# Optimization experiments

Measured on AMD Instinct MI355X. Metric: run time of the kernel, lower is better.

The kernel has to match this reference:

```python
import jax, jax.numpy as jnp
import numpy as np

PRE_NMS_TOP_K = 6000   # 'test' mode
POST_NMS_TOP_K = 300   # 'test' mode
IOU_THRESHOLD = 0.7


def setup_inputs() -> dict:
    key = jax.random.key(0)
    k1, k2, k3, k4 = jax.random.split(key, 4)
    B, A, H, W = 1, 9, 64, 96
    N = H * W * A  # 55296 anchors
    pred_cls = jax.random.normal(k1, (B, 2 * A, H, W), dtype=jnp.float32)
    pred_loc = jax.random.normal(k2, (B, 4 * A, H, W), dtype=jnp.float32) * 0.1
    # anchors in normalized (cx, cy, w, h) format
    cxcy = jax.random.uniform(k3, (N, 2), dtype=jnp.float32)
    wh = jax.random.uniform(k4, (N, 2), dtype=jnp.float32) * 0.2 + 0.02
    anchor = jnp.concatenate([cxcy, wh], axis=-1)
    return {"pred_cls": pred_cls, "pred_loc": pred_loc, "anchor": anchor}


def _decode_to_xy(loc, anchor):
    # decode: t(cx,cy) * a(w,h) + a(cx,cy); exp(t(w,h)) * a(w,h); then cxcy -> xyxy
    cxcy = loc[:, :2] * anchor[:, 2:] + anchor[:, :2]
    wh = jnp.exp(loc[:, 2:]) * anchor[:, 2:]
    return jnp.concatenate([cxcy - wh * 0.5, cxcy + wh * 0.5], axis=-1)


def _iou_matrix(boxes):
    # boxes: [N,4] xyxy -> [N,N] IoU
    area = (boxes[:, 2] - boxes[:, 0]) * (boxes[:, 3] - boxes[:, 1])
    lt = jnp.maximum(boxes[:, None, :2], boxes[None, :, :2])  # [N,N,2]
    rb = jnp.minimum(boxes[:, None, 2:], boxes[None, :, 2:])  # [N,N,2]
    wh = jnp.clip(rb - lt, 0.0)
    inter = wh[..., 0] * wh[..., 1]
    union = area[:, None] + area[None, :] - inter
    return inter / jnp.maximum(union, 1e-12)


def _nms_keep(boxes, iou_threshold):
    # boxes already sorted by descending score -> greedy NMS
    n = boxes.shape[0]
    iou = _iou_matrix(boxes)
    idx = jnp.arange(n)

    def body(i, keep):
        suppress = (iou[i] > iou_threshold) & (idx > i)
        return jnp.where(keep[i], keep & ~suppress, keep)

    return jax.lax.fori_loop(0, n, body, jnp.ones((n,), dtype=bool))


def reference(pred_cls, pred_loc, anchor):
    B = pred_cls.shape[0]
    # NCHW -> NHWC -> [N, 2] / [N, 4]  (batch squeezed, B == 1)
    cls = jnp.transpose(pred_cls, (0, 2, 3, 1)).reshape(B, -1, 2)[0]
    loc = jnp.transpose(pred_loc, (0, 2, 3, 1)).reshape(B, -1, 4)[0]

    roi = jnp.clip(_decode_to_xy(loc, anchor), 0.0, 1.0)           # [N,4]
    scores = jax.nn.sigmoid(cls)[:, 1]                              # [N]

    order = jnp.argsort(-scores)[:PRE_NMS_TOP_K]                    # descending
    roi = roi[order]                                                # [K,4]

    keep = _nms_keep(roi, IOU_THRESHOLD)                            # [K] bool
    # kept boxes first (stable -> preserves score order), take top 300
    sel = jnp.argsort(jnp.where(keep, 0, 1), stable=True)[:POST_NMS_TOP_K]
    valid = keep[sel]
    # pad with zeros if fewer than 300 boxes survive NMS (torch returns a
    # dynamically-sized tensor; we keep a fixed [300,4] with zero padding)
    return jnp.where(valid[:, None], roi[sel], 0.0)
```

## Files before the change

### kernel.cpp

```cpp
#include <hip/hip_runtime.h>


#define ADIM 9
#define NANCH 55296
#define HWSZ 6144
#define CH_U4 1536
#define TOT_U4 13824
#define SAMP_U4 3456
#define TOPK 6000
#define OUTK 300
#define NBINS 16384
#define CAP 8192
#define SCAP 1024
#define SRANK 128
#define MROWS 512
#define MW 8
#define THR 0.7f

typedef unsigned long long u64;
typedef unsigned int u32;

__device__ __forceinline__ u32 flipu(u32 b) {
    u32 u = (b & 0x80000000u) ? ~b : (b | 0x80000000u);
    return ~u;
}

__device__ __forceinline__ bool iou_gt(float4 a, float aa, float4 b, float ba) {
    float ix = fminf(a.z, b.z) - fmaxf(a.x, b.x);
    float iy = fminf(a.w, b.w) - fmaxf(a.y, b.y);
    float inter = fmaxf(ix, 0.f) * fmaxf(iy, 0.f);
    float u = fmaxf(aa + ba - inter, 1e-12f);
    float d = __builtin_fmaf(-THR, u, inter);
    if (__builtin_fabsf(d) > 1e-6f * u) return d > 0.f;
    return inter / u > THR;
}

__device__ __forceinline__ float4 decode_box(const float* __restrict__ loc,
                                             const float* __restrict__ anc, u32 n) {
    u32 a = n % 9u, hw = n / 9u;
    float t0 = loc[(4 * a + 0) * HWSZ + hw];
    float t1 = loc[(4 * a + 1) * HWSZ + hw];
    float t2 = loc[(4 * a + 2) * HWSZ + hw];
    float t3 = loc[(4 * a + 3) * HWSZ + hw];
    float4 an = reinterpret_cast<const float4*>(anc)[n];
    float cx = t0 * an.z + an.x;
    float cy = t1 * an.w + an.y;
    float bw = expf(t2) * an.z;
    float bh = expf(t3) * an.w;
    return make_float4(fminf(fmaxf(cx - bw * 0.5f, 0.f), 1.f),
                       fminf(fmaxf(cy - bh * 0.5f, 0.f), 1.f),
                       fminf(fmaxf(cx + bw * 0.5f, 0.f), 1.f),
                       fminf(fmaxf(cy + bh * 0.5f, 0.f), 1.f));
}

__device__ __forceinline__ u64 sx64(u64 v, int m) {
    u32 lo = __shfl_xor((u32)(v & 0xffffffffu), m, 64);
    u32 hi = __shfl_xor((u32)(v >> 32), m, 64);
    return ((u64)hi << 32) | lo;
}

__device__ __forceinline__ u64 ce64(u64 v, int j, int lane, bool up) {
    u64 pv = sx64(v, j);
    u64 mn = (pv < v) ? pv : v;
    u64 mx = (pv < v) ? v : pv;
    return (((lane & j) == 0) == up) ? mn : mx;
}

__device__ __forceinline__ uint4 ld_cls4(const uint4* __restrict__ cls4, int i) {
    int ch = i / CH_U4;
    int e4 = i - ch * CH_U4;
    return cls4[(2 * ch + 1) * CH_U4 + e4];
}

__device__ __forceinline__ u32 block_scan(u32 s, int wid, int lane, u32* wsum) {
    u32 x = s;
    #pragma unroll
    for (int d = 1; d < 64; d <<= 1) {
        u32 y = __shfl_up(x, (unsigned)d, 64);
        if (lane >= d) x += y;
    }
    if (lane == 63) wsum[wid] = x;
    __syncthreads();
    if (wid == 0) {
        u32 w = (lane < 16) ? wsum[lane] : 0u;
        #pragma unroll
        for (int d = 1; d < 16; d <<= 1) {
            u32 y = __shfl_up(w, (unsigned)d, 64);
            if (lane >= d) w += y;
        }
        if (lane < 16) wsum[lane] = w;
    }
    __syncthreads();
    return x + (wid ? wsum[wid - 1] : 0u);
}

__device__ __forceinline__ u32 find_cutoff(const u32* hist, u32 thresh, int tid,
                                           int wid, int lane, u32* wsum, u32* sB) {
    u32 h[16];
    const uint4* h4 = reinterpret_cast<const uint4*>(hist);
    #pragma unroll
    for (int k = 0; k < 4; ++k) {
        uint4 v = h4[tid * 4 + k];
        h[4 * k + 0] = v.x; h[4 * k + 1] = v.y; h[4 * k + 2] = v.z; h[4 * k + 3] = v.w;
    }
    u32 s = 0;
    #pragma unroll
    for (int b = 0; b < 16; ++b) s += h[b];
    u32 incl = block_scan(s, wid, lane, wsum);
    u32 before = incl - s;
    if (before < thresh && incl >= thresh) {
        u32 run = before;
        #pragma unroll
        for (int b = 0; b < 16; ++b) {
            run += h[b];
            if (run >= thresh) { sB[0] = (u32)(tid * 16 + b); break; }
        }
    }
    __syncthreads();
    u32 r = sB[0];
    __syncthreads();
    return r;
}

__global__ void __launch_bounds__(1024) k_scan(const float* __restrict__ cls,
                                               u32* __restrict__ wsSfs,
                                               u32* __restrict__ wsSidx,
                                               u32* __restrict__ wsMeta) {
    __shared__ u32 hist[NBINS];
    __shared__ __align__(16) u32 sfs[SCAP];
    __shared__ u32 sidx[SCAP];
    __shared__ u32 wsum[16];
    __shared__ u32 sB[2];
    __shared__ u32 shu[2];

    const int tid = threadIdx.x;
    const int wid = tid >> 6;
    const int lane = tid & 63;
    const uint4* cls4 = reinterpret_cast<const uint4*>(cls);

    u64* h64 = (u64*)hist;
    for (int i = tid; i < NBINS / 2; i += 1024) h64[i] = 0ull;
    if (tid < 2) shu[tid] = 0;
    __syncthreads();
    {
        uint4 s0 = ld_cls4(cls4, 4 * tid);
        uint4 s1 = ld_cls4(cls4, 4 * (tid + 1024));
        uint4 s2 = ld_cls4(cls4, 4 * (tid + 2048));
        bool has3 = tid < (SAMP_U4 - 3072);
        uint4 s3 = has3 ? ld_cls4(cls4, 4 * (tid + 3072)) : make_uint4(0u,0u,0u,0u);
        atomicAdd(&hist[flipu(s0.x) >> 18], 1u); atomicAdd(&hist[flipu(s0.y) >> 18], 1u);
        atomicAdd(&hist[flipu(s0.z) >> 18], 1u); atomicAdd(&hist[flipu(s0.w) >> 18], 1u);
        atomicAdd(&hist[flipu(s1.x) >> 18], 1u); atomicAdd(&hist[flipu(s1.y) >> 18], 1u);
        atomicAdd(&hist[flipu(s1.z) >> 18], 1u); atomicAdd(&hist[flipu(s1.w) >> 18], 1u);
        atomicAdd(&hist[flipu(s2.x) >> 18], 1u); atomicAdd(&hist[flipu(s2.y) >> 18], 1u);
        atomicAdd(&hist[flipu(s2.z) >> 18], 1u); atomicAdd(&hist[flipu(s2.w) >> 18], 1u);
        if (has3) {
            atomicAdd(&hist[flipu(s3.x) >> 18], 1u); atomicAdd(&hist[flipu(s3.y) >> 18], 1u);
            atomicAdd(&hist[flipu(s3.z) >> 18], 1u); atomicAdd(&hist[flipu(s3.w) >> 18], 1u);
        }
    }
    __syncthreads();
    const u32 B1 = find_cutoff(hist, SRANK, tid, wid, lane, wsum, sB);
    const u32 K1 = (B1 + 1u) << 18;

    u64 bm = 0;
    u32 cnt = 0;
    #pragma unroll
    for (int half = 0; half < 2; ++half) {
        uint4 buf[7];
        #pragma unroll
        for (int kk = 0; kk < 7; ++kk) {
            int i = (half * 7 + kk) * 1024 + tid;
            buf[kk] = (i < TOT_U4) ? ld_cls4(cls4, i) : make_uint4(0xFFFFFFFFu,0xFFFFFFFFu,0xFFFFFFFFu,0xFFFFFFFFu);
        }
        #pragma unroll
        for (int kk = 0; kk < 7; ++kk) {
            int i = (half * 7 + kk) * 1024 + tid;
            if (i < TOT_U4) {
                #pragma unroll
                for (int c = 0; c < 4; ++c) {
                    u32 b = (c == 0) ? buf[kk].x : (c == 1) ? buf[kk].y
                          : (c == 2) ? buf[kk].z : buf[kk].w;
                    if (flipu(b) < K1) {
                        cnt++;
                        bm |= 1ull << ((half * 7 + kk) * 4 + c);
                    }
                }
            }
        }
    }
    u32 incl = block_scan(cnt, wid, lane, wsum);
    u32 base = incl - cnt;
    if (tid == 1023) shu[0] = incl;
    __syncthreads();
    const u32 csRaw = shu[0];
    const u32 cs = csRaw < SCAP ? csRaw : SCAP;
    if (csRaw <= SCAP) {
        u64 m = bm;
        u32 o = base;
        while (m) {
            int b = __ffsll((unsigned long long)m) - 1;
            m &= m - 1;
            int kk = b >> 2, c = b & 3;
            int i = kk * 1024 + tid;
            uint4 v = ld_cls4(cls4, i);
            u32 raw = (c == 0) ? v.x : (c == 1) ? v.y : (c == 2) ? v.z : v.w;
            int ch = i / CH_U4;
            int e4 = i - ch * CH_U4;
            u32 n = (u32)((e4 * 4 + c) * ADIM + ch);
            if (o < SCAP) { sfs[o] = flipu(raw); sidx[o] = n; }
            o++;
        }
    }
    if (tid >= (int)cs) { sfs[tid] = 0xFFFFFFFFu; sidx[tid] = 0xFFFFFFFFu; }
    __syncthreads();
    wsSfs[tid] = sfs[tid];
    wsSidx[tid] = sidx[tid];
    if (tid == 0) { wsMeta[0] = csRaw; wsMeta[1] = B1; }
}

__global__ void __launch_bounds__(1024) k_rank(const float* __restrict__ loc,
                                               const float* __restrict__ anc,
                                               const u32* __restrict__ wsSfs,
                                               const u32* __restrict__ wsSidx,
                                               const u32* __restrict__ wsMeta,
                                               float4* __restrict__ boxS,
                                               float* __restrict__ areaS) {
    __shared__ u32 Lfs[SCAP];
    __shared__ u32 Lidx[SCAP];
    const int tid = threadIdx.x;
    const u32 csRaw = wsMeta[0];
    if (csRaw > SCAP) return;

    Lfs[tid] = wsSfs[tid];
    Lidx[tid] = wsSidx[tid];
    __syncthreads();

    const int ci = blockIdx.x * 64 + (tid >> 4);
    const int p = tid & 15;
    const u32 myf = Lfs[ci];
    const u32 myi = Lidx[ci];
    u32 r = 0;
    #pragma unroll 8
    for (int k = 0; k < 64; ++k) {
        int j = k * 16 + p;
        u32 fj = Lfs[j];
        u32 ij = Lidx[j];
        r += (fj < myf) || (fj == myf && ij < myi);
    }
    r += __shfl_xor(r, 1, 64);
    r += __shfl_xor(r, 2, 64);
    r += __shfl_xor(r, 4, 64);
    r += __shfl_xor(r, 8, 64);
    if (p == 0 && (u32)ci < csRaw) {
        float4 b = decode_box(loc, anc, myi);
        boxS[r] = b;
        areaS[r] = (b.z - b.x) * (b.w - b.y);
    }
}

__global__ void __launch_bounds__(1024) k_mat(const u32* __restrict__ wsMeta,
                                              const float4* __restrict__ boxS,
                                              const float* __restrict__ areaS,
                                              u32* __restrict__ maskG32) {
    __shared__ float4 B[MROWS];
    __shared__ float  A[MROWS];
    __shared__ u32 M32[32][16];
    const int tid = threadIdx.x;
    const u32 csRaw = wsMeta[0];
    if (csRaw > SCAP) return;
    const u32 rowsv = csRaw < MROWS ? csRaw : MROWS;

    if (tid < MROWS) { B[tid] = boxS[tid]; A[tid] = areaS[tid]; }
    if (tid < 512) M32[tid >> 4][tid & 15] = 0u;
    __syncthreads();

    const int rl = tid >> 5;
    const int sub = tid & 31;
    const int row = blockIdx.x + 16 * rl;
    if (row < (int)rowsv) {
        const int j0 = sub * 16;
        int jmax = row < j0 + 16 ? row : j0 + 16;
        if (j0 < jmax) {
            float4 rb = B[row];
            float rba = A[row];
            u32 bits = 0;
            #pragma unroll 4
            for (int j = j0; j < jmax; ++j)
                if (iou_gt(rb, rba, B[j], A[j])) bits |= 1u << (j - j0);
            if (bits) atomicOr(&M32[rl][sub >> 1], bits << ((sub & 1) * 16));
        }
    }
    __syncthreads();
    if (tid < 512) {
        int rl2 = tid >> 4, w = tid & 15;
        int row2 = blockIdx.x + 16 * rl2;
        maskG32[row2 * 16 + w] = M32[rl2][w];
    }
}

__global__ void __launch_bounds__(1024) k_greedy(const float* __restrict__ cls,
                                                 const float* __restrict__ loc,
                                                 const float* __restrict__ anc,
                                                 const u32* __restrict__ wsMeta,
                                                 const float4* __restrict__ boxS,
                                                 const float* __restrict__ areaS,
                                                 const u32* __restrict__ maskG32,
                                                 float4* __restrict__ out) {
    __shared__ u64 cand[CAP];
    __shared__ u64 smask[MROWS][MW];
    __shared__ float4 sbox[SCAP];
    __shared__ float  sarea[SCAP];
    __shared__ float4 kept[OUTK];
    __shared__ float  karea[OUTK];
    __shared__ float4 cbox[64];
    __shared__ float  carea[64];
    __shared__ u64 supw[16];
    __shared__ u64 sbyp[1024];
    __shared__ u32 wsum[16];
    __shared__ u32 sB[2];
    __shared__ u32 shu[8];

    const int tid = threadIdx.x;
    const int wid = tid >> 6;
    const int lane = tid & 63;
    u32* hist = (u32*)cand;
    const uint4* cls4 = reinterpret_cast<const uint4*>(cls);

    const u32 csRaw = wsMeta[0];
    const u32 cs = csRaw < SCAP ? csRaw : SCAP;
    const bool fast = (csRaw <= SCAP);

    if (tid < 8) shu[tid] = 0;
    sbox[tid] = boxS[tid];
    sarea[tid] = areaS[tid];
    {
        u32* sm32 = (u32*)smask;
        #pragma unroll
        for (int k = 0; k < 8; ++k) sm32[k * 1024 + tid] = maskG32[k * 1024 + tid];
    }
    __syncthreads();

    if (fast) {
        const u32 rowsv = cs < MROWS ? cs : MROWS;
        if (wid == 0) {
            u32 kc = 0, nexti0 = 0;
            u64 K[MW];
            #pragma unroll
            for (int w = 0; w < MW; ++w) K[w] = 0ull;
            #pragma unroll
            for (int cw = 0; cw < MW; ++cw) {
                u32 i0 = (u32)cw * 64u;
                if (i0 < rowsv && kc < OUTK) {
                    u32 ci = i0 + (u32)lane;
                    bool valid = ci < rowsv;
                    u64 myw[MW];
                    #pragma unroll
                    for (int w = 0; w < MW; ++w) myw[w] = valid ? smask[ci][w] : 0ull;
                    u64 supk = 0;
                    #pragma unroll
                    for (int w = 0; w < MW; ++w) supk |= myw[w] & K[w];
                    bool ia = valid && (supk == 0ull);
                    u64 inch = myw[cw] & ((1ull << lane) - 1ull);
                    u64 A = __ballot(ia ? 1 : 0);
                    for (int itx = 0; itx < 64; ++itx) {
                        bool na = ia && ((inch & A) == 0ull);
                        u64 A2 = __ballot(na ? 1 : 0);
                        if (A2 == A) break;
                        A = A2;
                    }
                    bool kp = (A >> lane) & 1;
                    u32 rank = (u32)__popcll(A & ((1ull << lane) - 1ull));
                    if (kp && kc + rank < OUTK) {
                        float4 c = sbox[ci];
                        kept[kc + rank] = c;
                        karea[kc + rank] = sarea[ci];
                        out[kc + rank] = c;
                    }
                    K[cw] = A;
                    kc += (u32)__popcll(A);
                    nexti0 = i0 + 64;
                }
            }
            if (lane == 0) {
                shu[4] = kc > OUTK ? OUTK : kc;
                shu[5] = nexti0;
            }
        }

        const u32 limit = cs;
        while (true) {
            __syncthreads();
            u32 kc = shu[4], i0 = shu[5];
            if (kc >= OUTK || i0 >= limit) break;
            u32 ci = i0 + (u32)lane;
            bool valid = ci < limit;
            float4 c = sbox[valid ? ci : 0];
            float ca = sarea[valid ? ci : 0];

            bool sup = false;
            for (u32 j = (u32)wid; j < kc; j += 16)
                sup = sup || iou_gt(c, ca, kept[j], karea[j]);
            u64 bal = __ballot(sup ? 1 : 0);
            if (lane == 0) supw[wid] = bal;

            u64 sby = 0;
            u32 smax = 4u * wid + 4u; if (smax > 63u) smax = 63u;
            for (u32 s = 4u * wid + 1u; s <= smax; ++s) {
                u32 p = ((u32)lane + s) & 63u;
                if (p < (u32)lane && (i0 + p) < limit)
                    if (iou_gt(c, ca, sbox[i0 + p], sarea[i0 + p])) sby |= (1ull << p);
            }
            sbyp[wid * 64 + lane] = sby;
            __syncthreads();

            if (wid == 0) {
                u64 sup64 = 0, sbyfull = 0;
                #pragma unroll
                for (int w = 0; w < 16; ++w) { sup64 |= supw[w]; sbyfull |= sbyp[w * 64 + lane]; }
                bool ia = valid && !((sup64 >> lane) & 1);
                u64 A = __ballot(ia ? 1 : 0);
                for (int itx = 0; itx < 64; ++itx) {
                    bool na = ia && ((sbyfull & A) == 0);
                    u64 A2 = __ballot(na ? 1 : 0);
                    if (A2 == A) break;
                    A = A2;
                }
                bool kp = (A >> lane) & 1;
                u32 rank = (u32)__popcll(A & ((1ull << lane) - 1ull));
                if (kp && kc + rank < OUTK) {
                    kept[kc + rank] = c; karea[kc + rank] = ca; out[kc + rank] = c;
                }
                if (lane == 0) {
                    u32 nk = kc + (u32)__popcll(A);
                    shu[4] = nk > OUTK ? OUTK : nk;
                    shu[5] = i0 + 64;
                }
            }
        }
    }

    __syncthreads();
    if (shu[4] < OUTK) {
        const u32 consumed = fast ? cs : 0u;
        u64* h64 = (u64*)hist;
        for (int i = tid; i < NBINS / 2; i += 1024) h64[i] = 0ull;
        __syncthreads();
        #pragma unroll
        for (int half = 0; half < 2; ++half) {
            uint4 buf[7];
            #pragma unroll
            for (int kk = 0; kk < 7; ++kk) {
                int i = (half * 7 + kk) * 1024 + tid;
                buf[kk] = (i < TOT_U4) ? ld_cls4(cls4, i) : make_uint4(0u,0u,0u,0u);
            }
            #pragma unroll
            for (int kk = 0; kk < 7; ++kk) {
                int i = (half * 7 + kk) * 1024 + tid;
                if (i < TOT_U4) {
                    atomicAdd(&hist[flipu(buf[kk].x) >> 18], 1u);
                    atomicAdd(&hist[flipu(buf[kk].y) >> 18], 1u);
                    atomicAdd(&hist[flipu(buf[kk].z) >> 18], 1u);
                    atomicAdd(&hist[flipu(buf[kk].w) >> 18], 1u);
                }
            }
        }
        __syncthreads();
        const u32 B2 = find_cutoff(hist, TOPK, tid, wid, lane, wsum, sB);
        u64 bm2 = 0;
        u32 cnt2 = 0;
        #pragma unroll
        for (int half = 0; half < 2; ++half) {
            uint4 buf[7];
            #pragma unroll
            for (int kk = 0; kk < 7; ++kk) {
                int i = (half * 7 + kk) * 1024 + tid;
                buf[kk] = (i < TOT_U4) ? ld_cls4(cls4, i) : make_uint4(0xFFFFFFFFu,0xFFFFFFFFu,0xFFFFFFFFu,0xFFFFFFFFu);
            }
            #pragma unroll
            for (int kk = 0; kk < 7; ++kk) {
                int i = (half * 7 + kk) * 1024 + tid;
                if (i < TOT_U4) {
                    #pragma unroll
                    for (int c = 0; c < 4; ++c) {
                        u32 b = (c == 0) ? buf[kk].x : (c == 1) ? buf[kk].y
                              : (c == 2) ? buf[kk].z : buf[kk].w;
                        if ((flipu(b) >> 18) <= B2) {
                            cnt2++;
                            bm2 |= 1ull << ((half * 7 + kk) * 4 + c);
                        }
                    }
                }
            }
        }
        __syncthreads();
        for (int i = tid; i < CAP; i += 1024) cand[i] = ~0ull;
        u32 incl2 = block_scan(cnt2, wid, lane, wsum);
        u32 base2 = incl2 - cnt2;
        if (tid == 1023) shu[1] = incl2;
        __syncthreads();
        {
            u64 m2 = bm2;
            u32 o = base2;
            while (m2) {
                int b = __ffsll((unsigned long long)m2) - 1;
                m2 &= m2 - 1;
                int kk = b >> 2, c = b & 3;
                int i = kk * 1024 + tid;
                uint4 v = ld_cls4(cls4, i);
                u32 raw = (c == 0) ? v.x : (c == 1) ? v.y : (c == 2) ? v.z : v.w;
                int ch = i / CH_U4;
                int e4 = i - ch * CH_U4;
                u32 n = (u32)((e4 * 4 + c) * ADIM + ch);
                if (o < CAP) cand[o] = ((u64)flipu(raw) << 32) | n;
                o++;
            }
        }
        __syncthreads();
        const u32 totF = shu[1];
        const u32 limfb = totF < TOPK ? totF : TOPK;
        for (int seg = wid; seg < CAP / 64; seg += 16) {
            u64 v = cand[seg * 64 + lane];
            #pragma unroll
            for (int k = 2; k <= 64; k <<= 1)
                #pragma unroll
                for (int j = k >> 1; j >= 1; j >>= 1)
                    v = ce64(v, j, lane, (((seg * 64 + lane) & k) == 0));
            cand[seg * 64 + lane] = v;
        }
        __syncthreads();
        for (int k = 128; k <= CAP; k <<= 1) {
            for (int j = k >> 1; j >= 64; j >>= 1) {
                for (u32 p = (u32)tid; p < CAP / 2; p += 1024) {
                    u32 i = ((p & ~(u32)(j - 1)) << 1) | (p & (u32)(j - 1));
                    u32 l = i | (u32)j;
                    bool up = ((i & (u32)k) == 0);
                    u64 a = cand[i], b = cand[l];
                    if ((a > b) == up) { cand[i] = b; cand[l] = a; }
                }
                __syncthreads();
            }
            for (int seg = wid; seg < CAP / 64; seg += 16) {
                u64 v = cand[seg * 64 + lane];
                bool up = (((seg * 64) & k) == 0);
                #pragma unroll
                for (int j = 32; j >= 1; j >>= 1) v = ce64(v, j, lane, up);
                cand[seg * 64 + lane] = v;
            }
            __syncthreads();
        }
        if (tid == 0) shu[5] = consumed;
        while (true) {
            __syncthreads();
            u32 kc = shu[4], i0 = shu[5];
            if (kc >= OUTK || i0 >= limfb) break;
            if (wid == 0) {
                u32 ci = i0 + (u32)lane;
                u32 n = (ci < limfb) ? (u32)cand[ci] : 0u;
                float4 b = decode_box(loc, anc, n);
                cbox[lane] = b;
                carea[lane] = (b.z - b.x) * (b.w - b.y);
            }
            __syncthreads();
            u32 ci = i0 + (u32)lane;
            bool valid = ci < limfb;
            float4 c = cbox[lane];
            float ca = carea[lane];
            bool sup = false;
            for (u32 j = (u32)wid; j < kc; j += 16)
                sup = sup || iou_gt(c, ca, kept[j], karea[j]);
            u64 bal = __ballot(sup ? 1 : 0);
            if (lane == 0) supw[wid] = bal;
            u64 sby = 0;
            u32 smax = 4u * wid + 4u; if (smax > 63u) smax = 63u;
            for (u32 s = 4u * wid + 1u; s <= smax; ++s) {
                u32 p = ((u32)lane + s) & 63u;
                if (p < (u32)lane && (i0 + p) < limfb)
                    if (iou_gt(c, ca, cbox[p], carea[p])) sby |= (1ull << p);
            }
            sbyp[wid * 64 + lane] = sby;
            __syncthreads();
            if (wid == 0) {
                u64 sup64 = 0, sbyfull = 0;
                #pragma unroll
                for (int w = 0; w < 16; ++w) { sup64 |= supw[w]; sbyfull |= sbyp[w * 64 + lane]; }
                bool ia = valid && !((sup64 >> lane) & 1);
                u64 A = __ballot(ia ? 1 : 0);
                for (int itx = 0; itx < 64; ++itx) {
                    bool na = ia && ((sbyfull & A) == 0);
                    u64 A2 = __ballot(na ? 1 : 0);
                    if (A2 == A) break;
                    A = A2;
                }
                bool kp = (A >> lane) & 1;
                u32 rank = (u32)__popcll(A & ((1ull << lane) - 1ull));
                if (kp && kc + rank < OUTK) {
                    kept[kc + rank] = c; karea[kc + rank] = ca; out[kc + rank] = c;
                }
                if (lane == 0) {
                    u32 nk = kc + (u32)__popcll(A);
                    shu[4] = nk > OUTK ? OUTK : nk;
                    shu[5] = i0 + 64;
                }
            }
        }
    }

    __syncthreads();
    u32 kc = shu[4];
    for (u32 r = (u32)tid; r < OUTK; r += 1024)
        if (r >= kc) out[r] = make_float4(0.f, 0.f, 0.f, 0.f);
}

extern "C" void kernel_launch(void* const* d_in, const int* in_sizes, int n_in,
                              void* d_out, int out_size, void* d_ws, size_t ws_size,
                              hipStream_t stream) {
    const float* cls = (const float*)d_in[0];
    const float* loc = (const float*)d_in[1];
    const float* anc = (const float*)d_in[2];

    char* ws = (char*)d_ws;
    u32*    wsSfs   = (u32*)(ws + 0);
    u32*    wsSidx  = (u32*)(ws + 4096);
    u32*    wsMeta  = (u32*)(ws + 8192);
    float4* boxS    = (float4*)(ws + 8208);
    float*  areaS   = (float*)(ws + 24592);
    u32*    maskG32 = (u32*)(ws + 28688);

    k_scan  <<<1, 1024, 0, stream>>>(cls, wsSfs, wsSidx, wsMeta);
    k_rank  <<<16, 1024, 0, stream>>>(loc, anc, wsSfs, wsSidx, wsMeta, boxS, areaS);
    k_mat   <<<16, 1024, 0, stream>>>(wsMeta, boxS, areaS, maskG32);
    k_greedy<<<1, 1024, 0, stream>>>(cls, loc, anc, wsMeta, boxS, areaS, maskG32, (float4*)d_out);
}
```

Baseline: 36.69 us.

## Fuse scan and rank kernels by recomputing the scan in every block

Merges the single-block candidate scan kernel and the 16-block rank kernel into one kernel launched with 16 blocks. Each block redundantly recomputes the histogram and candidate compaction, then ranks its own 64-candidate slice straight from shared memory. This removes one kernel launch and the global round trip of the candidate arrays. The cost is 16 copies of the full scan work competing for memory bandwidth.

```diff
diff --git a/kernel.cpp b/kernel.cpp
--- a/kernel.cpp
+++ b/kernel.cpp
@@ -122,10 +122,12 @@
     return r;
 }
 
-__global__ void __launch_bounds__(1024) k_scan(const float* __restrict__ cls,
-                                               u32* __restrict__ wsSfs,
-                                               u32* __restrict__ wsSidx,
-                                               u32* __restrict__ wsMeta) {
+__global__ void __launch_bounds__(1024) k_scanrank(const float* __restrict__ cls,
+                                                   const float* __restrict__ loc,
+                                                   const float* __restrict__ anc,
+                                                   u32* __restrict__ wsMeta,
+                                                   float4* __restrict__ boxS,
+                                                   float* __restrict__ areaS) {
     __shared__ u32 hist[NBINS];
     __shared__ __align__(16) u32 sfs[SCAP];
     __shared__ u32 sidx[SCAP];
@@ -195,7 +197,10 @@
     __syncthreads();
     const u32 csRaw = shu[0];
     const u32 cs = csRaw < SCAP ? csRaw : SCAP;
-    if (csRaw <= SCAP) {
+    if (blockIdx.x == 0 && tid == 0) { wsMeta[0] = csRaw; wsMeta[1] = B1; }
+    if (csRaw > SCAP) return;
+
+    {
         u64 m = bm;
         u32 o = base;
         while (m) {
@@ -214,38 +219,17 @@
     }
     if (tid >= (int)cs) { sfs[tid] = 0xFFFFFFFFu; sidx[tid] = 0xFFFFFFFFu; }
     __syncthreads();
-    wsSfs[tid] = sfs[tid];
-    wsSidx[tid] = sidx[tid];
-    if (tid == 0) { wsMeta[0] = csRaw; wsMeta[1] = B1; }
-}
-
-__global__ void __launch_bounds__(1024) k_rank(const float* __restrict__ loc,
-                                               const float* __restrict__ anc,
-                                               const u32* __restrict__ wsSfs,
-                                               const u32* __restrict__ wsSidx,
-                                               const u32* __restrict__ wsMeta,
-                                               float4* __restrict__ boxS,
-                                               float* __restrict__ areaS) {
-    __shared__ u32 Lfs[SCAP];
-    __shared__ u32 Lidx[SCAP];
-    const int tid = threadIdx.x;
-    const u32 csRaw = wsMeta[0];
-    if (csRaw > SCAP) return;
-
-    Lfs[tid] = wsSfs[tid];
-    Lidx[tid] = wsSidx[tid];
-    __syncthreads();
 
     const int ci = blockIdx.x * 64 + (tid >> 4);
     const int p = tid & 15;
-    const u32 myf = Lfs[ci];
-    const u32 myi = Lidx[ci];
+    const u32 myf = sfs[ci];
+    const u32 myi = sidx[ci];
     u32 r = 0;
     #pragma unroll 8
     for (int k = 0; k < 64; ++k) {
         int j = k * 16 + p;
-        u32 fj = Lfs[j];
-        u32 ij = Lidx[j];
+        u32 fj = sfs[j];
+        u32 ij = sidx[j];
         r += (fj < myf) || (fj == myf && ij < myi);
     }
     r += __shfl_xor(r, 1, 64);
@@ -620,15 +604,12 @@
     const float* anc = (const float*)d_in[2];
 
     char* ws = (char*)d_ws;
-    u32*    wsSfs   = (u32*)(ws + 0);
-    u32*    wsSidx  = (u32*)(ws + 4096);
-    u32*    wsMeta  = (u32*)(ws + 8192);
-    float4* boxS    = (float4*)(ws + 8208);
-    float*  areaS   = (float*)(ws + 24592);
-    u32*    maskG32 = (u32*)(ws + 28688);
-
-    k_scan  <<<1, 1024, 0, stream>>>(cls, wsSfs, wsSidx, wsMeta);
-    k_rank  <<<16, 1024, 0, stream>>>(loc, anc, wsSfs, wsSidx, wsMeta, boxS, areaS);
-    k_mat   <<<16, 1024, 0, stream>>>(wsMeta, boxS, areaS, maskG32);
-    k_greedy<<<1, 1024, 0, stream>>>(cls, loc, anc, wsMeta, boxS, areaS, maskG32, (float4*)d_out);
-}
+    u32*    wsMeta  = (u32*)(ws + 0);
+    float4* boxS    = (float4*)(ws + 16);
+    float*  areaS   = (float*)(ws + 16400);
+    u32*    maskG32 = (u32*)(ws + 20496);
+
+    k_scanrank<<<16, 1024, 0, stream>>>(cls, loc, anc, wsMeta, boxS, areaS);
+    k_mat     <<<16, 1024, 0, stream>>>(wsMeta, boxS, areaS, maskG32);
+    k_greedy  <<<1, 1024, 0, stream>>>(cls, loc, anc, wsMeta, boxS, areaS, maskG32, (float4*)d_out);
+}
```

Result: faster. 35.00 us (-4.6%).
